# Kernel optimization log

Measured on AMD Instinct MI355X. Metric: run time of the kernel, lower is better.

Reference implementation:

```python
import jax, jax.numpy as jnp
import numpy as np

H = 16        # num_attention_heads
DH = 64       # attention_head_dim
D = H * DH    # model dim = 1024
FF = 4 * D    # feed-forward inner dim = 4096
SCALE = DH ** -0.5
EPS = 1e-12


def _ln(x, g, b):
    m = jnp.mean(x, axis=-1, keepdims=True)
    v = jnp.mean((x - m) ** 2, axis=-1, keepdims=True)
    return (x - m) * jax.lax.rsqrt(v + EPS) * g + b


def _attn(x, ctx, Wq, Wk, Wv, Wo, bo, mask):
    # x: [B,S,D] (already pre-normed), ctx: [B,T,D], mask: [B,T] int (1=keep) or None
    B, S, _ = x.shape
    T = ctx.shape[1]
    q = (x @ Wq).reshape(B, S, H, DH)
    k = (ctx @ Wk).reshape(B, T, H, DH)
    v = (ctx @ Wv).reshape(B, T, H, DH)
    scores = jnp.einsum('bqhd,bkhd->bhqk', q, k) * SCALE  # [B,H,S,T]
    if mask is not None:
        scores = jnp.where(mask[:, None, None, :] == 0, -jnp.inf, scores)
    probs = jax.nn.softmax(scores, axis=-1)
    out = jnp.einsum('bhqk,bkhd->bqhd', probs, v).reshape(B, S, D)
    return out @ Wo + bo


def _geglu_ff(x, Wff1, bff1, Wff2, bff2):
    y = x @ Wff1 + bff1                 # [B,S,2*FF]
    h, gate = y[..., :FF], y[..., FF:]
    # GEGLU computes exact (erf) gelu in fp32
    g = jax.nn.gelu(gate.astype(jnp.float32), approximate=False).astype(gate.dtype)
    return (h * g) @ Wff2 + bff2


def setup_inputs() -> dict:
    key = jax.random.key(0)
    ks = jax.random.split(key, 24)
    B, S, T = 4, 1024, 1024
    w = lambda k, shp: jax.random.normal(k, shp, dtype=jnp.float32) * 0.02
    inp = {
        'hidden_states': jax.random.normal(ks[0], (B, S, D), dtype=jnp.float32),
        'context': jax.random.normal(ks[1], (B, T, D), dtype=jnp.float32),
        'encoder_key_padding_mask': jnp.ones((B, T), dtype=jnp.int32),
        'g1': jnp.ones((D,), jnp.float32), 'b1': jnp.zeros((D,), jnp.float32),
        'g2': jnp.ones((D,), jnp.float32), 'b2': jnp.zeros((D,), jnp.float32),
        'g3': jnp.ones((D,), jnp.float32), 'b3': jnp.zeros((D,), jnp.float32),
        'Wq1': w(ks[2], (D, D)), 'Wk1': w(ks[3], (D, D)), 'Wv1': w(ks[4], (D, D)),
        'Wo1': w(ks[5], (D, D)), 'bo1': jnp.zeros((D,), jnp.float32),
        'Wq2': w(ks[6], (D, D)), 'Wk2': w(ks[7], (D, D)), 'Wv2': w(ks[8], (D, D)),
        'Wo2': w(ks[9], (D, D)), 'bo2': jnp.zeros((D,), jnp.float32),
        'Wff1': w(ks[10], (D, 2 * FF)), 'bff1': jnp.zeros((2 * FF,), jnp.float32),
        'Wff2': w(ks[11], (FF, D)), 'bff2': jnp.zeros((D,), jnp.float32),
    }
    return inp


def reference(hidden_states, context, encoder_key_padding_mask,
              g1, b1, g2, b2, g3, b3,
              Wq1, Wk1, Wv1, Wo1, bo1,
              Wq2, Wk2, Wv2, Wo2, bo2,
              Wff1, bff1, Wff2, bff2):
    # Self-attention (attn1): context defaults to (normed) hidden_states, no padding mask
    n1 = _ln(hidden_states, g1, b1)
    h = hidden_states + _attn(n1, n1, Wq1, Wk1, Wv1, Wo1, bo1, None)
    # Cross-attention (attn2) with encoder key padding mask
    n2 = _ln(h, g2, b2)
    h = h + _attn(n2, context, Wq2, Wk2, Wv2, Wo2, bo2, encoder_key_padding_mask)
    # GEGLU feed-forward
    h = h + _geglu_ff(_ln(h, g3, b3), Wff1, bff1, Wff2, bff2)
    return h
```

## Files before the change

### kernel.cpp

```cpp
#include <hip/hip_runtime.h>

typedef unsigned short u16;
typedef unsigned int u32;

#define B_ 4
#define S_ 1024
#define D_ 1024
#define H_ 16
#define DH_ 64
#define FF_ 4096
#define M_ 4096
#define SCALE_ 0.125f

typedef __attribute__((ext_vector_type(8))) __bf16 bf16x8;
typedef __attribute__((ext_vector_type(4))) float f32x4;

__device__ __forceinline__ f32x4 mfma16(bf16x8 a, bf16x8 b, f32x4 c) {
  return __builtin_amdgcn_mfma_f32_16x16x32_bf16(a, b, c, 0, 0, 0);
}

__device__ __forceinline__ u16 f2bf(float x) {
  union { __bf16 h; u16 u; } cv; cv.h = (__bf16)x; return cv.u;
}
__device__ __forceinline__ float bf2f(u16 u) {
  union { u32 u; float f; } cv; cv.u = ((u32)u) << 16; return cv.f;
}
__device__ __forceinline__ u32 packbf2(float a, float b) {
  union { u32 u; __bf16 h[2]; } pk;
  pk.h[0] = (__bf16)a; pk.h[1] = (__bf16)b;
  return pk.u;
}
__device__ __forceinline__ float gelu_exact(float x) {
  return 0.5f * x * (1.f + erff(x * 0.7071067811865475f));
}
__device__ __forceinline__ void gload16(const void* g, void* l) {
  __builtin_amdgcn_global_load_lds((__attribute__((address_space(1))) void*)(g),
                                   (__attribute__((address_space(3))) void*)(l),
                                   16, 0, 0);
}

template<int EPI>
__global__ __launch_bounds__(256, 2) void gemm128(
    const u16* __restrict__ A, const u16* __restrict__ BT,
    const float* __restrict__ bias, const float* __restrict__ res,
    void* __restrict__ out, int M, int N, int K, int ktiles)
{
  __shared__ u16 As[2][128 * 64];
  __shared__ u16 Bs[2][128 * 64];

  const int tid = threadIdx.x;
  const int wave = tid >> 6, lane = tid & 63;
  const int wm = wave >> 1, wn = wave & 1;
  const int qi = lane & 15, g = lane >> 4;

  const int gx = N >> 7;
  const int nwg = gx * (M >> 7);
  int id = blockIdx.y * gridDim.x + blockIdx.x;
  id = (id & 7) * (nwg >> 3) + (id >> 3);
  const int m0 = (id / gx) << 7, n0 = (id % gx) << 7;

  const int NT = ktiles;
  const int kbase = blockIdx.z * ktiles * 64;

  const int r0 = tid >> 3;
  const int scol = (((tid & 7) ^ ((tid >> 3) & 7)) << 3);
  const int swb = wave << 6;

  f32x4 acc[4][4];
#pragma unroll
  for (int i = 0; i < 4; ++i)
#pragma unroll
    for (int j = 0; j < 4; ++j)
      acc[i][j] = (f32x4){0.f, 0.f, 0.f, 0.f};

#define STAGE_A(t, h, b) {                                                  \
    const int tt = (t) >= NT ? (t) - NT : (t);                              \
    _Pragma("unroll")                                                       \
    for (int i = 0; i < 2; ++i) {                                           \
      const int r = (h) * 64 + i * 32 + r0;                                 \
      gload16(A + (size_t)(m0 + r) * K + kbase + tt * 64 + scol,            \
              &As[b][(h) * 4096 + (i * 256 + swb) * 8]);                    \
    } }
#define STAGE_B(t, h, b) {                                                  \
    const int tt = (t) >= NT ? (t) - NT : (t);                              \
    _Pragma("unroll")                                                       \
    for (int i = 0; i < 2; ++i) {                                           \
      const int r = (h) * 64 + i * 32 + r0;                                 \
      gload16(BT + (size_t)(n0 + r) * K + kbase + tt * 64 + scol,           \
              &Bs[b][(h) * 4096 + (i * 256 + swb) * 8]);                    \
    } }

  bf16x8 af[4][2], bfr[4][2];

#define RD_ALL(b)                                                            \
  _Pragma("unroll") for (int mi = 0; mi < 4; ++mi)                           \
  _Pragma("unroll") for (int kk = 0; kk < 2; ++kk) {                         \
    const int row = wm * 64 + mi * 16 + qi;                                  \
    const int cb = ((kk * 64 + (g << 4)) ^ ((qi & 7) << 4));                 \
    af[mi][kk] = *(const bf16x8*)((const char*)&As[b][0] + row * 128 + cb);  \
  }                                                                          \
  _Pragma("unroll") for (int ni = 0; ni < 4; ++ni)                           \
  _Pragma("unroll") for (int kk = 0; kk < 2; ++kk) {                         \
    const int row = wn * 64 + ni * 16 + qi;                                  \
    const int cb = ((kk * 64 + (g << 4)) ^ ((qi & 7) << 4));                 \
    bfr[ni][kk] = *(const bf16x8*)((const char*)&Bs[b][0] + row * 128 + cb); \
  }

#define HALF(milo)                                                           \
  _Pragma("unroll") for (int mi = (milo); mi < (milo) + 2; ++mi)             \
  _Pragma("unroll") for (int ni = 0; ni < 4; ++ni)                           \
  _Pragma("unroll") for (int kk = 0; kk < 2; ++kk)                           \
    acc[mi][ni] = mfma16(af[mi][kk], bfr[ni][kk], acc[mi][ni]);

#define BAR() __builtin_amdgcn_s_barrier()
#define LGKM0() { asm volatile("s_waitcnt lgkmcnt(0)" ::: "memory");         \
                  __builtin_amdgcn_sched_barrier(0); }
#define VM8() asm volatile("s_waitcnt vmcnt(8)" ::: "memory")
#define PRIO(x) __builtin_amdgcn_s_setprio(x)

  STAGE_A(0, 0, 0); STAGE_A(0, 1, 0); STAGE_B(0, 0, 0); STAGE_B(0, 1, 0);
  STAGE_A(1, 0, 1); STAGE_A(1, 1, 1); STAGE_B(1, 0, 1); STAGE_B(1, 1, 1);
  VM8();
  BAR();

  const int NI = NT >> 1;
  for (int it = 0; it < NI; ++it) {
    const int k = it * 2;
    RD_ALL(0); LGKM0();
    BAR();
    STAGE_A(k + 2, 0, 0); STAGE_A(k + 2, 1, 0);
    PRIO(1); HALF(0); PRIO(0);
    STAGE_B(k + 2, 0, 0); STAGE_B(k + 2, 1, 0);
    PRIO(1); HALF(2); PRIO(0);
    VM8();
    BAR();
    RD_ALL(1); LGKM0();
    BAR();
    STAGE_A(k + 3, 0, 1); STAGE_A(k + 3, 1, 1);
    PRIO(1); HALF(0); PRIO(0);
    STAGE_B(k + 3, 0, 1); STAGE_B(k + 3, 1, 1);
    PRIO(1); HALF(2); PRIO(0);
    VM8();
    BAR();
  }

#pragma unroll
  for (int mi = 0; mi < 4; ++mi) {
#pragma unroll
    for (int ni = 0; ni < 4; ++ni) {
#pragma unroll
      for (int r = 0; r < 4; ++r) {
        const int m = m0 + wm * 64 + mi * 16 + g * 4 + r;
        const int n = n0 + wn * 64 + ni * 16 + qi;
        float v = acc[mi][ni][r];
        if (EPI == 0 || EPI == 5) {
          const int ts = n >> 10, b = m >> 10, s = m & 1023;
          const int hh = (n >> 6) & 15, dh = n & 63;
          if (EPI == 0 && ts == 0) v *= SCALE_;
          ((u16*)out)[(size_t)ts * (B_ * H_ * S_ * DH_) +
                      (((size_t)(b * H_ + hh) * S_) + s) * DH_ + dh] = f2bf(v);
        } else {
          const size_t idx = (size_t)m * N + n;
          ((float*)out)[idx] = res[idx] + v + bias[n];
        }
      }
    }
  }
#undef STAGE_A
#undef STAGE_B
#undef RD_ALL
#undef HALF
#undef BAR
#undef LGKM0
#undef VM8
#undef PRIO
}

__global__ __launch_bounds__(256, 2) void ffgeglu(
    const u16* __restrict__ A, const u16* __restrict__ BTh,
    const u16* __restrict__ BTg, const float* __restrict__ bias,
    u16* __restrict__ out)
{
  __shared__ u16 As[128 * 64];
  __shared__ u16 Bhs[128 * 64];
  __shared__ u16 Bgs[128 * 64];

  const int tid = threadIdx.x;
  const int wave = tid >> 6, lane = tid & 63;
  const int wm = wave >> 1, wn = wave & 1;
  const int qi = lane & 15, g = lane >> 4;

  const int orig = blockIdx.y * gridDim.x + blockIdx.x;
  const int c = orig & 7, j = orig >> 3;
  const int cm = c >> 2, cn = c & 3;
  const int jm = j & 15, jn = j >> 4;
  const int m0 = (cm * 16 + jm) << 7;
  const int n0 = (cn * 8 + jn) << 7;
  const int K = 1024;

  const int r0 = tid >> 3;
  const int scol = (((tid & 7) ^ ((tid >> 3) & 7)) << 3);
  const int swb = wave << 6;

  f32x4 acch[4][4], accg[4][4];
#pragma unroll
  for (int i = 0; i < 4; ++i)
#pragma unroll
    for (int j2 = 0; j2 < 4; ++j2) {
      acch[i][j2] = (f32x4){0.f, 0.f, 0.f, 0.f};
      accg[i][j2] = (f32x4){0.f, 0.f, 0.f, 0.f};
    }

  for (int t = 0; t < 16; ++t) {
    if (t) __syncthreads();
#pragma unroll
    for (int i = 0; i < 4; ++i) {
      const int r = i * 32 + r0;
      gload16(A + (size_t)(m0 + r) * K + t * 64 + scol,
              &As[(i * 256 + swb) * 8]);
    }
#pragma unroll
    for (int i = 0; i < 4; ++i) {
      const int r = i * 32 + r0;
      gload16(BTh + (size_t)(n0 + r) * K + t * 64 + scol,
              &Bhs[(i * 256 + swb) * 8]);
    }
#pragma unroll
    for (int i = 0; i < 4; ++i) {
      const int r = i * 32 + r0;
      gload16(BTg + (size_t)(n0 + r) * K + t * 64 + scol,
              &Bgs[(i * 256 + swb) * 8]);
    }
    __syncthreads();

    bf16x8 af[4][2], bfr[4][2];
#pragma unroll
    for (int mi = 0; mi < 4; ++mi)
#pragma unroll
      for (int kk = 0; kk < 2; ++kk) {
        const int row = wm * 64 + mi * 16 + qi;
        const int cb = ((kk * 64 + (g << 4)) ^ ((qi & 7) << 4));
        af[mi][kk] = *(const bf16x8*)((const char*)&As[0] + row * 128 + cb);
      }
#pragma unroll
    for (int ni = 0; ni < 4; ++ni)
#pragma unroll
      for (int kk = 0; kk < 2; ++kk) {
        const int row = wn * 64 + ni * 16 + qi;
        const int cb = ((kk * 64 + (g << 4)) ^ ((qi & 7) << 4));
        bfr[ni][kk] = *(const bf16x8*)((const char*)&Bhs[0] + row * 128 + cb);
      }
#pragma unroll
    for (int mi = 0; mi < 4; ++mi)
#pragma unroll
      for (int ni = 0; ni < 4; ++ni)
#pragma unroll
        for (int kk = 0; kk < 2; ++kk)
          acch[mi][ni] = mfma16(af[mi][kk], bfr[ni][kk], acch[mi][ni]);
#pragma unroll
    for (int ni = 0; ni < 4; ++ni)
#pragma unroll
      for (int kk = 0; kk < 2; ++kk) {
        const int row = wn * 64 + ni * 16 + qi;
        const int cb = ((kk * 64 + (g << 4)) ^ ((qi & 7) << 4));
        bfr[ni][kk] = *(const bf16x8*)((const char*)&Bgs[0] + row * 128 + cb);
      }
#pragma unroll
    for (int mi = 0; mi < 4; ++mi)
#pragma unroll
      for (int ni = 0; ni < 4; ++ni)
#pragma unroll
        for (int kk = 0; kk < 2; ++kk)
          accg[mi][ni] = mfma16(af[mi][kk], bfr[ni][kk], accg[mi][ni]);
  }

#pragma unroll
  for (int mi = 0; mi < 4; ++mi) {
#pragma unroll
    for (int ni = 0; ni < 4; ++ni) {
#pragma unroll
      for (int r = 0; r < 4; ++r) {
        const int m = m0 + wm * 64 + mi * 16 + g * 4 + r;
        const int n = n0 + wn * 64 + ni * 16 + qi;
        const float hv = acch[mi][ni][r] + bias[n];
        const float gv = accg[mi][ni][r] + bias[FF_ + n];
        out[(size_t)m * FF_ + n] = f2bf(hv * gelu_exact(gv));
      }
    }
  }
}

template<bool MASKED>
__global__ __launch_bounds__(256, 4) void attn_kernel(
    const u16* __restrict__ Q, const u16* __restrict__ Kb,
    const u16* __restrict__ VT, const float* __restrict__ bias,
    u16* __restrict__ O, int S, int T)
{
  __shared__ u16 Ks[64 * 72];
  __shared__ u16 VTs[64 * 72];
  __shared__ u16 Ps[4][16 * 72];
  __shared__ float biasS[64];

  const int bh = blockIdx.y;
  const int b = bh >> 4, h = bh & 15;
  const int tid = threadIdx.x;
  const int wave = tid >> 6, lane = tid & 63;
  const int g = lane >> 4, qi = lane & 15;
  const int q0w = blockIdx.x * 64 + wave * 16;

  const u16* Qb = Q + (size_t)bh * S * DH_;
  const u16* Kg = Kb + (size_t)bh * T * DH_;
  const u16* Vg = VT + (size_t)bh * DH_ * T;

  bf16x8 qf[2];
  qf[0] = *(const bf16x8*)&Qb[(q0w + qi) * DH_ + g * 8];
  qf[1] = *(const bf16x8*)&Qb[(q0w + qi) * DH_ + 32 + g * 8];

  f32x4 acc[4];
#pragma unroll
  for (int i = 0; i < 4; ++i) acc[i] = (f32x4){0.f, 0.f, 0.f, 0.f};
  float l_run = 1e-30f;

  u16* Pw = &Ps[wave][0];

  for (int t0 = 0; t0 < T; t0 += 64) {
    __syncthreads();
#pragma unroll
    for (int i = 0; i < 2; ++i) {
      const int flat = i * 256 + tid;
      const int row = flat >> 3, kc = flat & 7;
      *(uint4*)&Ks[row * 72 + kc * 8] = *(const uint4*)&Kg[(size_t)(t0 + row) * DH_ + kc * 8];
      *(uint4*)&VTs[row * 72 + kc * 8] = *(const uint4*)&Vg[(size_t)row * T + t0 + kc * 8];
    }
    if (MASKED && tid < 64) biasS[tid] = bias[b * T + t0 + tid];
    __syncthreads();

    f32x4 sacc[4];
#pragma unroll
    for (int nt = 0; nt < 4; ++nt) sacc[nt] = (f32x4){0.f, 0.f, 0.f, 0.f};
#pragma unroll
    for (int kk = 0; kk < 2; ++kk) {
#pragma unroll
      for (int nt = 0; nt < 4; ++nt) {
        bf16x8 kf = *(const bf16x8*)&Ks[(nt * 16 + qi) * 72 + kk * 32 + g * 8];
        sacc[nt] = mfma16(kf, qf[kk], sacc[nt]);
      }
    }
    float p[4][4];
    float lsum = 0.f;
#pragma unroll
    for (int nt = 0; nt < 4; ++nt)
#pragma unroll
      for (int r = 0; r < 4; ++r) {
        float v = sacc[nt][r];
        if (MASKED) v += biasS[nt * 16 + g * 4 + r];
        const float e = __expf(v);
        p[nt][r] = e;
        lsum += e;
      }
    lsum += __shfl_xor(lsum, 16);
    lsum += __shfl_xor(lsum, 32);
    l_run += lsum;

#pragma unroll
    for (int nt = 0; nt < 4; ++nt) {
      uint2 w;
      w.x = packbf2(p[nt][0], p[nt][1]);
      w.y = packbf2(p[nt][2], p[nt][3]);
      *(uint2*)&Pw[qi * 72 + nt * 16 + g * 4] = w;
    }

#pragma unroll
    for (int kk = 0; kk < 2; ++kk) {
      bf16x8 pf = *(const bf16x8*)&Pw[qi * 72 + kk * 32 + g * 8];
#pragma unroll
      for (int ndh = 0; ndh < 4; ++ndh) {
        bf16x8 vf = *(const bf16x8*)&VTs[(ndh * 16 + qi) * 72 + kk * 32 + g * 8];
        acc[ndh] = mfma16(vf, pf, acc[ndh]);
      }
    }
  }

  const float inv = 1.f / l_run;
  const int qg = q0w + qi;
#pragma unroll
  for (int ndh = 0; ndh < 4; ++ndh) {
    uint2 w;
    w.x = packbf2(acc[ndh][0] * inv, acc[ndh][1] * inv);
    w.y = packbf2(acc[ndh][2] * inv, acc[ndh][3] * inv);
    *(uint2*)&O[(size_t)(b * S_ + qg) * D_ + h * DH_ + ndh * 16 + g * 4] = w;
  }
}

__global__ __launch_bounds__(256) void ln_kernel(
    const float* __restrict__ x, const float* __restrict__ gg,
    const float* __restrict__ bb, u16* __restrict__ out)
{
  __shared__ float red[8];
  const int row = blockIdx.x, tid = threadIdx.x;
  const float4 v = ((const float4*)(x + (size_t)row * D_))[tid];
  float s = v.x + v.y + v.z + v.w;
  float sq = v.x * v.x + v.y * v.y + v.z * v.z + v.w * v.w;
#pragma unroll
  for (int m = 32; m; m >>= 1) {
    s += __shfl_xor(s, m);
    sq += __shfl_xor(sq, m);
  }
  const int wave = tid >> 6, lane = tid & 63;
  if (lane == 0) { red[wave * 2] = s; red[wave * 2 + 1] = sq; }
  __syncthreads();
  const float St = red[0] + red[2] + red[4] + red[6];
  const float SQt = red[1] + red[3] + red[5] + red[7];
  const float mean = St * (1.f / 1024.f);
  float var = SQt * (1.f / 1024.f) - mean * mean;
  var = fmaxf(var, 0.f);
  const float rinv = rsqrtf(var + 1e-12f);
  const float4 g4 = ((const float4*)gg)[tid];
  const float4 b4 = ((const float4*)bb)[tid];
  uint2 o;
  o.x = packbf2((v.x - mean) * rinv * g4.x + b4.x, (v.y - mean) * rinv * g4.y + b4.y);
  o.y = packbf2((v.z - mean) * rinv * g4.z + b4.z, (v.w - mean) * rinv * g4.w + b4.w);
  ((uint2*)(out + (size_t)row * D_))[tid] = o;
}

__global__ __launch_bounds__(256) void transpose_w(
    const float* __restrict__ in, u16* __restrict__ out, int K, int N)
{
  __shared__ float tile[32][33];
  const int tx = threadIdx.x & 31, ty = threadIdx.x >> 5;
  const int k0 = blockIdx.y * 32, n0 = blockIdx.x * 32;
#pragma unroll
  for (int j = 0; j < 4; ++j)
    tile[ty + 8 * j][tx] = in[(size_t)(k0 + ty + 8 * j) * N + n0 + tx];
  __syncthreads();
#pragma unroll
  for (int j = 0; j < 4; ++j)
    out[(size_t)(n0 + ty + 8 * j) * K + k0 + tx] = f2bf(tile[tx][ty + 8 * j]);
}

__global__ __launch_bounds__(256) void transpose_w8(
    const float* __restrict__ w0, const float* __restrict__ w1,
    const float* __restrict__ w2, const float* __restrict__ w3,
    const float* __restrict__ w4, const float* __restrict__ w5,
    const float* __restrict__ w6, const float* __restrict__ w7,
    u16* __restrict__ outbase)
{
  __shared__ float tile[32][33];
  const float* srcs[8] = {w0, w1, w2, w3, w4, w5, w6, w7};
  const float* in = srcs[blockIdx.z];
  u16* out = outbase + (size_t)blockIdx.z * 1024 * 1024;
  const int tx = threadIdx.x & 31, ty = threadIdx.x >> 5;
  const int k0 = blockIdx.y * 32, n0 = blockIdx.x * 32;
#pragma unroll
  for (int j = 0; j < 4; ++j)
    tile[ty + 8 * j][tx] = in[(size_t)(k0 + ty + 8 * j) * 1024 + n0 + tx];
  __syncthreads();
#pragma unroll
  for (int j = 0; j < 4; ++j)
    out[(size_t)(n0 + ty + 8 * j) * 1024 + k0 + tx] = f2bf(tile[tx][ty + 8 * j]);
}

__global__ __launch_bounds__(256) void transpose_v(
    const u16* __restrict__ in, u16* __restrict__ out, int T)
{
  __shared__ u16 tile[32][33];
  const int tx = threadIdx.x & 31, ty = threadIdx.x >> 5;
  const int bh = blockIdx.z;
  const int t0 = blockIdx.x * 32, d0 = blockIdx.y * 32;
  const u16* ib = in + (size_t)bh * T * DH_;
  u16* ob = out + (size_t)bh * DH_ * T;
#pragma unroll
  for (int j = 0; j < 4; ++j)
    tile[ty + 8 * j][tx] = ib[(size_t)(t0 + ty + 8 * j) * DH_ + d0 + tx];
  __syncthreads();
#pragma unroll
  for (int j = 0; j < 4; ++j)
    ob[(size_t)(d0 + ty + 8 * j) * T + t0 + tx] = tile[tx][ty + 8 * j];
}

__global__ void cvt_bf16(const float* __restrict__ in, u16* __restrict__ out, int n4)
{
  const int i = blockIdx.x * blockDim.x + threadIdx.x;
  if (i < n4) {
    const float4 v = ((const float4*)in)[i];
    uint2 o;
    o.x = packbf2(v.x, v.y);
    o.y = packbf2(v.z, v.w);
    ((uint2*)out)[i] = o;
  }
}

__global__ void mask_bias(const int* __restrict__ mask, float* __restrict__ bias, int n)
{
  const int i = blockIdx.x * blockDim.x + threadIdx.x;
  if (i < n) bias[i] = mask[i] ? 0.f : -1e30f;
}

extern "C" void kernel_launch(void* const* d_in, const int* in_sizes, int n_in,
                              void* d_out, int out_size, void* d_ws, size_t ws_size,
                              hipStream_t stream)
{
  (void)in_sizes; (void)n_in; (void)out_size; (void)ws_size;
  const float* hidden = (const float*)d_in[0];
  const float* ctx    = (const float*)d_in[1];
  const int*   mask   = (const int*)d_in[2];
  const float* g1 = (const float*)d_in[3];
  const float* b1 = (const float*)d_in[4];
  const float* g2 = (const float*)d_in[5];
  const float* b2 = (const float*)d_in[6];
  const float* g3 = (const float*)d_in[7];
  const float* b3 = (const float*)d_in[8];
  const float* Wq1 = (const float*)d_in[9];
  const float* Wk1 = (const float*)d_in[10];
  const float* Wv1 = (const float*)d_in[11];
  const float* Wo1 = (const float*)d_in[12];
  const float* bo1 = (const float*)d_in[13];
  const float* Wq2 = (const float*)d_in[14];
  const float* Wk2 = (const float*)d_in[15];
  const float* Wv2 = (const float*)d_in[16];
  const float* Wo2 = (const float*)d_in[17];
  const float* bo2 = (const float*)d_in[18];
  const float* Wff1 = (const float*)d_in[19];
  const float* bff1 = (const float*)d_in[20];
  const float* Wff2 = (const float*)d_in[21];
  const float* bff2 = (const float*)d_in[22];

  char* ws = (char*)d_ws;
  size_t off = 0;
  auto alloc = [&](size_t bytes) -> void* {
    void* p = ws + off;
    off += (bytes + 255) & ~(size_t)255;
    return p;
  };
  u16* WqT1  = (u16*)alloc((size_t)1024 * 1024 * 2);
  u16* WkT1  = (u16*)alloc((size_t)1024 * 1024 * 2);
  u16* WvT1  = (u16*)alloc((size_t)1024 * 1024 * 2);
  u16* WoT1  = (u16*)alloc((size_t)1024 * 1024 * 2);
  u16* WqT2  = (u16*)alloc((size_t)1024 * 1024 * 2);
  u16* WkT2  = (u16*)alloc((size_t)1024 * 1024 * 2);
  u16* WvT2  = (u16*)alloc((size_t)1024 * 1024 * 2);
  u16* WoT2  = (u16*)alloc((size_t)1024 * 1024 * 2);
  u16* Wff1T = (u16*)alloc((size_t)8192 * 1024 * 2);
  u16* Wff2T = (u16*)alloc((size_t)1024 * 4096 * 2);
  u16* nbuf  = (u16*)alloc((size_t)M_ * D_ * 2);
  u16* hgbuf = (u16*)alloc((size_t)M_ * FF_ * 2);
  u16* qbuf  = (u16*)alloc((size_t)M_ * D_ * 2);
  u16* kbuf  = (u16*)alloc((size_t)M_ * D_ * 2);
  u16* vbuf  = (u16*)alloc((size_t)M_ * D_ * 2);
  u16* vtbuf = (u16*)alloc((size_t)M_ * D_ * 2);
  u16* attnb = (u16*)alloc((size_t)M_ * D_ * 2);
  u16* ctxb  = (u16*)alloc((size_t)M_ * D_ * 2);
  float* biasw = (float*)alloc((size_t)B_ * S_ * 4);
  float* hres = (float*)d_out;
  (void)WkT1; (void)WvT1; (void)WkT2; (void)WvT2; (void)WoT2;

  const dim3 blk(256);
  const dim3 gW8(32, 32, 8);
  const dim3 gQKV(24, 32);
  const dim3 gKV(16, 32);
  const dim3 gP(8, 32);
  const dim3 gFF(32, 32);
  const dim3 gA(16, 64);
  const dim3 gV(32, 2, 64);

  transpose_w8<<<gW8, blk, 0, stream>>>(Wq1, Wk1, Wv1, Wo1, Wq2, Wk2, Wv2, Wo2,
                                        WqT1);
  transpose_w<<<dim3(256, 32), blk, 0, stream>>>(Wff1, Wff1T, 1024, 8192);
  transpose_w<<<dim3(32, 128), blk, 0, stream>>>(Wff2, Wff2T, 4096, 1024);
  cvt_bf16<<<dim3(4096), blk, 0, stream>>>(ctx, ctxb, 1048576);
  mask_bias<<<dim3(16), blk, 0, stream>>>(mask, biasw, B_ * S_);

  ln_kernel<<<dim3(M_), blk, 0, stream>>>(hidden, g1, b1, nbuf);
  gemm128<0><<<gQKV, blk, 0, stream>>>(nbuf, WqT1, nullptr, nullptr,
                                       qbuf, M_, 3072, 1024, 16);
  transpose_v<<<gV, blk, 0, stream>>>(vbuf, vtbuf, 1024);
  attn_kernel<false><<<gA, blk, 0, stream>>>(qbuf, kbuf, vtbuf, nullptr, attnb,
                                             S_, S_);
  gemm128<1><<<gP, blk, 0, stream>>>(attnb, WoT1, bo1, hidden,
                                     hres, M_, 1024, 1024, 16);
  ln_kernel<<<dim3(M_), blk, 0, stream>>>(hres, g2, b2, nbuf);

  gemm128<0><<<gP, blk, 0, stream>>>(nbuf, WqT2, nullptr, nullptr,
                                     qbuf, M_, 1024, 1024, 16);
  gemm128<5><<<gKV, blk, 0, stream>>>(ctxb, WkT2, nullptr, nullptr,
                                      kbuf, M_, 2048, 1024, 16);
  transpose_v<<<gV, blk, 0, stream>>>(vbuf, vtbuf, 1024);
  attn_kernel<true><<<gA, blk, 0, stream>>>(qbuf, kbuf, vtbuf, biasw, attnb,
                                            S_, S_);
  gemm128<1><<<gP, blk, 0, stream>>>(attnb, WoT2, bo2, hres,
                                     hres, M_, 1024, 1024, 16);
  ln_kernel<<<dim3(M_), blk, 0, stream>>>(hres, g3, b3, nbuf);

  ffgeglu<<<gFF, blk, 0, stream>>>(nbuf, Wff1T, Wff1T + (size_t)FF_ * 1024,
                                   bff1, hgbuf);
  gemm128<1><<<gP, blk, 0, stream>>>(hgbuf, Wff2T, bff2, hres,
                                     hres, M_, 1024, 4096, 64);
}
```

Measured before the change: 359.2 us.

## Software-pipeline GEGLU GEMM with double-buffered B tiles and async prefetch

Restructures the FF1 GEGLU GEMM main loop so that the B (h and gate) tiles are double-buffered and the next tiles are prefetched while MFMAs run. The loads for step t+1 (A) and t+2 (B) are issued between the h and gate MFMA phases, with explicit vmcnt/lgkmcnt waits, raw barriers and setprio around the MFMA blocks. This is meant to hide global-to-LDS load latency that the old load-sync-compute loop exposed. It uses more LDS (five 16KB tiles instead of three), which may reduce occupancy, and it depends on hand-placed wait counts being correct. The wraparound index loads redundant tiles at the end of the loop.

```diff
diff --git a/kernel.cpp b/kernel.cpp
--- a/kernel.cpp
+++ b/kernel.cpp
@@ -182,8 +182,8 @@
     u16* __restrict__ out)
 {
   __shared__ u16 As[128 * 64];
-  __shared__ u16 Bhs[128 * 64];
-  __shared__ u16 Bgs[128 * 64];
+  __shared__ u16 Bhs[2][128 * 64];
+  __shared__ u16 Bgs[2][128 * 64];
 
   const int tid = threadIdx.x;
   const int wave = tid >> 6, lane = tid & 63;
@@ -197,6 +197,7 @@
   const int m0 = (cm * 16 + jm) << 7;
   const int n0 = (cn * 8 + jn) << 7;
   const int K = 1024;
+  const int NT = 16;
 
   const int r0 = tid >> 3;
   const int scol = (((tid & 7) ^ ((tid >> 3) & 7)) << 3);
@@ -211,67 +212,78 @@
       accg[i][j2] = (f32x4){0.f, 0.f, 0.f, 0.f};
     }
 
-  for (int t = 0; t < 16; ++t) {
-    if (t) __syncthreads();
-#pragma unroll
-    for (int i = 0; i < 4; ++i) {
-      const int r = i * 32 + r0;
-      gload16(A + (size_t)(m0 + r) * K + t * 64 + scol,
-              &As[(i * 256 + swb) * 8]);
-    }
-#pragma unroll
-    for (int i = 0; i < 4; ++i) {
-      const int r = i * 32 + r0;
-      gload16(BTh + (size_t)(n0 + r) * K + t * 64 + scol,
-              &Bhs[(i * 256 + swb) * 8]);
-    }
-#pragma unroll
-    for (int i = 0; i < 4; ++i) {
-      const int r = i * 32 + r0;
-      gload16(BTg + (size_t)(n0 + r) * K + t * 64 + scol,
-              &Bgs[(i * 256 + swb) * 8]);
-    }
-    __syncthreads();
-
-    bf16x8 af[4][2], bfr[4][2];
-#pragma unroll
-    for (int mi = 0; mi < 4; ++mi)
-#pragma unroll
-      for (int kk = 0; kk < 2; ++kk) {
-        const int row = wm * 64 + mi * 16 + qi;
-        const int cb = ((kk * 64 + (g << 4)) ^ ((qi & 7) << 4));
-        af[mi][kk] = *(const bf16x8*)((const char*)&As[0] + row * 128 + cb);
-      }
-#pragma unroll
-    for (int ni = 0; ni < 4; ++ni)
-#pragma unroll
-      for (int kk = 0; kk < 2; ++kk) {
-        const int row = wn * 64 + ni * 16 + qi;
-        const int cb = ((kk * 64 + (g << 4)) ^ ((qi & 7) << 4));
-        bfr[ni][kk] = *(const bf16x8*)((const char*)&Bhs[0] + row * 128 + cb);
-      }
-#pragma unroll
-    for (int mi = 0; mi < 4; ++mi)
-#pragma unroll
-      for (int ni = 0; ni < 4; ++ni)
-#pragma unroll
-        for (int kk = 0; kk < 2; ++kk)
-          acch[mi][ni] = mfma16(af[mi][kk], bfr[ni][kk], acch[mi][ni]);
-#pragma unroll
-    for (int ni = 0; ni < 4; ++ni)
-#pragma unroll
-      for (int kk = 0; kk < 2; ++kk) {
-        const int row = wn * 64 + ni * 16 + qi;
-        const int cb = ((kk * 64 + (g << 4)) ^ ((qi & 7) << 4));
-        bfr[ni][kk] = *(const bf16x8*)((const char*)&Bgs[0] + row * 128 + cb);
-      }
-#pragma unroll
-    for (int mi = 0; mi < 4; ++mi)
-#pragma unroll
-      for (int ni = 0; ni < 4; ++ni)
-#pragma unroll
-        for (int kk = 0; kk < 2; ++kk)
-          accg[mi][ni] = mfma16(af[mi][kk], bfr[ni][kk], accg[mi][ni]);
+#define FSTAGE_A(t) {                                                       \
+    const int tt = (t) >= NT ? (t) - NT : (t);                              \
+    _Pragma("unroll")                                                       \
+    for (int i = 0; i < 4; ++i) {                                           \
+      const int r = i * 32 + r0;                                            \
+      gload16(A + (size_t)(m0 + r) * K + tt * 64 + scol,                    \
+              &As[(i * 256 + swb) * 8]);                                    \
+    } }
+#define FSTAGE_BH(t, b) {                                                   \
+    const int tt = (t) >= NT ? (t) - NT : (t);                              \
+    _Pragma("unroll")                                                       \
+    for (int i = 0; i < 4; ++i) {                                           \
+      const int r = i * 32 + r0;                                            \
+      gload16(BTh + (size_t)(n0 + r) * K + tt * 64 + scol,                  \
+              &Bhs[b][(i * 256 + swb) * 8]);                                \
+    } }
+#define FSTAGE_BG(t, b) {                                                   \
+    const int tt = (t) >= NT ? (t) - NT : (t);                              \
+    _Pragma("unroll")                                                       \
+    for (int i = 0; i < 4; ++i) {                                           \
+      const int r = i * 32 + r0;                                            \
+      gload16(BTg + (size_t)(n0 + r) * K + tt * 64 + scol,                  \
+              &Bgs[b][(i * 256 + swb) * 8]);                                \
+    } }
+
+  bf16x8 af[4][2], bfr[4][2];
+
+#define FRD_A()                                                              \
+  _Pragma("unroll") for (int mi = 0; mi < 4; ++mi)                           \
+  _Pragma("unroll") for (int kk = 0; kk < 2; ++kk) {                         \
+    const int row = wm * 64 + mi * 16 + qi;                                  \
+    const int cb = ((kk * 64 + (g << 4)) ^ ((qi & 7) << 4));                 \
+    af[mi][kk] = *(const bf16x8*)((const char*)&As[0] + row * 128 + cb);     \
+  }
+#define FRD_B(base)                                                          \
+  _Pragma("unroll") for (int ni = 0; ni < 4; ++ni)                           \
+  _Pragma("unroll") for (int kk = 0; kk < 2; ++kk) {                         \
+    const int row = wn * 64 + ni * 16 + qi;                                  \
+    const int cb = ((kk * 64 + (g << 4)) ^ ((qi & 7) << 4));                 \
+    bfr[ni][kk] = *(const bf16x8*)((const char*)(base) + row * 128 + cb);    \
+  }
+#define FMFMA(accx)                                                          \
+  _Pragma("unroll") for (int mi = 0; mi < 4; ++mi)                           \
+  _Pragma("unroll") for (int ni = 0; ni < 4; ++ni)                           \
+  _Pragma("unroll") for (int kk = 0; kk < 2; ++kk)                           \
+    accx[mi][ni] = mfma16(af[mi][kk], bfr[ni][kk], accx[mi][ni]);
+
+#define BAR() __builtin_amdgcn_s_barrier()
+#define LGKM0() { asm volatile("s_waitcnt lgkmcnt(0)" ::: "memory");         \
+                  __builtin_amdgcn_sched_barrier(0); }
+#define VM8() asm volatile("s_waitcnt vmcnt(8)" ::: "memory")
+#define PRIO(x) __builtin_amdgcn_s_setprio(x)
+
+  FSTAGE_BH(0, 0); FSTAGE_BG(0, 0);
+  FSTAGE_A(0);
+  FSTAGE_BH(1, 1); FSTAGE_BG(1, 1);
+  VM8();
+  BAR();
+
+  for (int t = 0; t < NT; ++t) {
+    const int b = t & 1;
+    FRD_A();
+    FRD_B(&Bhs[b][0]);
+    PRIO(1); FMFMA(acch); PRIO(0);
+    FRD_B(&Bgs[b][0]);
+    LGKM0();
+    BAR();
+    FSTAGE_A(t + 1);
+    FSTAGE_BH(t + 2, b); FSTAGE_BG(t + 2, b);
+    PRIO(1); FMFMA(accg); PRIO(0);
+    VM8();
+    BAR();
   }
 
 #pragma unroll
@@ -288,6 +300,16 @@
       }
     }
   }
+#undef FSTAGE_A
+#undef FSTAGE_BH
+#undef FSTAGE_BG
+#undef FRD_A
+#undef FRD_B
+#undef FMFMA
+#undef BAR
+#undef LGKM0
+#undef VM8
+#undef PRIO
 }
 
 template<bool MASKED>
```

After: 371.5 us. 3.4% more time.
